# Kernel tuning notes

Hardware: AMD Instinct MI355X
Metric: run time of the kernel (lower is better)

## Reference

```python
import jax, jax.numpy as jnp
import numpy as np

B, S, E, H = 2, 2048, 1024, 16
D = E // H  # d_k = n_wires = 64


def setup_inputs() -> dict:
    key = jax.random.key(0)
    ks = jax.random.split(key, 6)
    x = jax.random.normal(ks[0], (B, S, E), dtype=jnp.float32)
    scale = 0.02
    Wq = jax.random.normal(ks[1], (E, E), dtype=jnp.float32) * scale
    Wk = jax.random.normal(ks[2], (E, E), dtype=jnp.float32) * scale
    Wv = jax.random.normal(ks[3], (E, E), dtype=jnp.float32) * scale
    Wc = jax.random.normal(ks[4], (E, E), dtype=jnp.float32) * scale
    bc = jnp.zeros((E,), dtype=jnp.float32)
    return {"x": x, "Wq": Wq, "Wk": Wk, "Wv": Wv, "Wc": Wc, "bc": bc}


def _split_heads(t):
    # [B,S,E] -> [B,H,S,D]
    return t.reshape(B, S, H, D).transpose(0, 2, 1, 3)


def _quantum(t):
    # RX(theta_i) per wire + CNOT ladder + per-wire PauliZ expectation:
    # <Z_j> = prod_{i<=j} cos(theta_i)  (closed form of the circuit)
    return jnp.cumprod(jnp.cos(t), axis=-1)


def reference(x, Wq, Wk, Wv, Wc, bc):
    q = _quantum(_split_heads(x @ Wq.T))  # [B,H,S,D]
    k = _quantum(_split_heads(x @ Wk.T))
    v = _quantum(_split_heads(x @ Wv.T))
    scores = jnp.einsum('bhsd,bhtd->bhst', q, k) / jnp.sqrt(jnp.float32(D))
    attn = jax.nn.softmax(scores, axis=-1)
    out = jnp.einsum('bhst,bhtd->bhsd', attn, v)  # [B,H,S,D]
    out = out.transpose(0, 2, 1, 3).reshape(B, S, E)
    return out @ Wc.T + bc
```

## Files before the change

kernel.cpp:

```cpp
#include <hip/hip_runtime.h>
#include <hip/hip_bf16.h>

constexpr int Bc = 2, Sc = 2048, Ec = 1024, Hc = 16, Dc = 64;
constexpr int Mrows = Bc * Sc;
constexpr int Kdim  = Ec;

typedef float  floatx4 __attribute__((ext_vector_type(4)));
typedef short  shortx8 __attribute__((ext_vector_type(8)));

__device__ inline unsigned short f2bf(float f) {
    union { __hip_bfloat16 h; unsigned short u; } cv;
    cv.h = __float2bfloat16(f);
    return cv.u;
}

__device__ inline float exp2_fast(float x) {
#if __has_builtin(__builtin_amdgcn_exp2f)
    return __builtin_amdgcn_exp2f(x);
#else
    return __expf(x * 0.69314718056f);
#endif
}

__global__ __launch_bounds__(256) void convert_all_kernel(
    const float* __restrict__ x,  const float* __restrict__ Wq,
    const float* __restrict__ Wk, const float* __restrict__ Wv,
    const float* __restrict__ Wc,
    unsigned short* __restrict__ xb,  unsigned short* __restrict__ Wqb,
    unsigned short* __restrict__ Wkb, unsigned short* __restrict__ Wvb,
    unsigned short* __restrict__ Wcb)
{
    const long t = (long)blockIdx.x * 256 + threadIdx.x;
    const long i = t * 4;
    const float* src; unsigned short* dst; long off;
    if (i < 4194304) { src = x; dst = xb; off = i; }
    else {
        long j = i - 4194304;
        int wsel = (int)(j >> 20);
        off = j & 1048575;
        src = (wsel == 0) ? Wq : (wsel == 1) ? Wk : (wsel == 2) ? Wv : Wc;
        dst = (wsel == 0) ? Wqb : (wsel == 1) ? Wkb : (wsel == 2) ? Wvb : Wcb;
    }
    float4 v = *(const float4*)(src + off);
    unsigned short tmp[4] __attribute__((aligned(8)));
    tmp[0] = f2bf(v.x); tmp[1] = f2bf(v.y); tmp[2] = f2bf(v.z); tmp[3] = f2bf(v.w);
    *(uint2*)(dst + off) = *(uint2*)tmp;
}

__global__ __launch_bounds__(256) void proj_mfma_kernel(
    const unsigned short* __restrict__ Ab,
    const unsigned short* __restrict__ Wqb,
    const unsigned short* __restrict__ Wkb,
    const unsigned short* __restrict__ Wvb,
    unsigned short* __restrict__ oq,
    unsigned short* __restrict__ ok,
    unsigned short* __restrict__ ov)
{
    __shared__ __align__(16) char smem[128 * 72 * 2 * 2];
    unsigned short (*As)[72] = (unsigned short(*)[72])smem;
    unsigned short (*Ws)[72] = (unsigned short(*)[72])(smem + 128 * 72 * 2);
    float (*Cs)[132] = (float(*)[132])smem;
    __shared__ float Sp[64][9];

    const int z = blockIdx.z;
    const unsigned short* Wb = (z == 0) ? Wqb : (z == 1) ? Wkb : Wvb;
    unsigned short* out      = (z == 0) ? oq  : (z == 1) ? ok  : ov;
    const int mode = (z == 2) ? 1 : 0;

    const int tid = threadIdx.x;
    const int w = tid >> 6, l15 = tid & 15, quad = (tid >> 4) & 3;
    const int wq = w >> 1, wn = w & 1;
    const int m0 = blockIdx.x * 128;
    const int n0 = blockIdx.y * 128;
    const int h0 = n0 >> 6;
    const int srow = tid >> 3, schk = tid & 7;

    floatx4 acc[4][4];
    #pragma unroll
    for (int ms = 0; ms < 4; ++ms)
        #pragma unroll
        for (int ns = 0; ns < 4; ++ns)
            #pragma unroll
            for (int e = 0; e < 4; ++e) acc[ms][ns][e] = 0.0f;

    for (int k0 = 0; k0 < Kdim; k0 += 64) {
        #pragma unroll
        for (int it = 0; it < 4; ++it) {
            int row = srow + 32 * it;
            *(shortx8*)&As[row][schk * 8] =
                *(const shortx8*)(Ab + (size_t)(m0 + row) * Kdim + k0 + schk * 8);
            *(shortx8*)&Ws[row][schk * 8] =
                *(const shortx8*)(Wb + (size_t)(n0 + row) * Kdim + k0 + schk * 8);
        }
        __syncthreads();
        #pragma unroll
        for (int ks = 0; ks < 2; ++ks) {
            shortx8 af[4], bf[4];
            #pragma unroll
            for (int ms = 0; ms < 4; ++ms)
                af[ms] = *(shortx8*)&As[64 * wq + 16 * ms + l15][32 * ks + 8 * quad];
            #pragma unroll
            for (int ns = 0; ns < 4; ++ns)
                bf[ns] = *(shortx8*)&Ws[64 * wn + 16 * ns + l15][32 * ks + 8 * quad];
            #pragma unroll
            for (int ms = 0; ms < 4; ++ms)
                #pragma unroll
                for (int ns = 0; ns < 4; ++ns)
                    acc[ms][ns] = __builtin_amdgcn_mfma_f32_16x16x32_bf16(
                        af[ms], bf[ns], acc[ms][ns], 0, 0, 0);
        }
        __syncthreads();
    }

    const int b = m0 >> 11;
    const int sbase = m0 & (Sc - 1);

    for (int pass = 0; pass < 2; ++pass) {
        if (wq == pass) {
            #pragma unroll
            for (int ms = 0; ms < 4; ++ms)
                #pragma unroll
                for (int ns = 0; ns < 4; ++ns)
                    #pragma unroll
                    for (int r = 0; r < 4; ++r)
                        Cs[16 * ms + 4 * quad + r][64 * wn + 16 * ns + l15] =
                            __cosf(acc[ms][ns][r]);
        }
        __syncthreads();
        #pragma unroll
        for (int t = tid; t < 512; t += 256) {
            int row = t >> 3, seg = t & 7;
            float pr = 1.0f;
            #pragma unroll
            for (int c = 0; c < 16; ++c) pr *= Cs[row][seg * 16 + c];
            Sp[row][seg] = pr;
        }
        __syncthreads();
        if (mode == 0) {
            #pragma unroll
            for (int t = tid; t < 512; t += 256) {
                int row = t >> 3, seg = t & 7;
                float p = 1.0f;
                for (int j = (seg & 4); j < seg; ++j) p *= Sp[row][j];
                unsigned short tmp[16] __attribute__((aligned(16)));
                #pragma unroll
                for (int c = 0; c < 16; ++c) { p *= Cs[row][seg * 16 + c]; tmp[c] = f2bf(p); }
                int h = h0 + (seg >> 2);
                int s = sbase + pass * 64 + row;
                size_t base = (((size_t)b * Hc + h) * Sc + s) * Dc + (seg & 3) * 16;
                *(shortx8*)(out + base)     = *(shortx8*)&tmp[0];
                *(shortx8*)(out + base + 8) = *(shortx8*)&tmp[8];
            }
            __syncthreads();
        } else {
            #pragma unroll
            for (int t = tid; t < 512; t += 256) {
                int row = t >> 3, seg = t & 7;
                float p = 1.0f;
                for (int j = (seg & 4); j < seg; ++j) p *= Sp[row][j];
                #pragma unroll
                for (int c = 0; c < 16; ++c) { p *= Cs[row][seg * 16 + c]; Cs[row][seg * 16 + c] = p; }
            }
            __syncthreads();
            #pragma unroll
            for (int t = tid; t < 512; t += 256) {
                int col = t >> 2, chunk = t & 3;
                int h = h0 + (col >> 6), d = col & 63;
                unsigned short tmp[16] __attribute__((aligned(16)));
                #pragma unroll
                for (int j = 0; j < 16; ++j) tmp[j] = f2bf(Cs[chunk * 16 + j][col]);
                size_t base = (((size_t)b * Hc + h) * Dc + d) * Sc
                              + sbase + pass * 64 + chunk * 16;
                *(shortx8*)(out + base)     = *(shortx8*)&tmp[0];
                *(shortx8*)(out + base + 8) = *(shortx8*)&tmp[8];
            }
            __syncthreads();
        }
    }
}

__global__ __launch_bounds__(256) void attn_mfma_kernel(
    const unsigned short* __restrict__ qg,
    const unsigned short* __restrict__ kg,
    const unsigned short* __restrict__ vtg,
    unsigned short* __restrict__ att)
{
    __shared__ __align__(16) unsigned short Ks[64][72];
    __shared__ __align__(16) unsigned short VTs[64][72];
    __shared__ __align__(16) unsigned short Pq[128][72];

    const int tid  = threadIdx.x;
    const int w    = tid >> 6;
    const int l15  = tid & 15;
    const int quad = (tid >> 4) & 3;
    const int qb   = blockIdx.x;
    const int bh   = blockIdx.y;

    const unsigned short* qp = qg  + (size_t)bh * Sc * Dc;
    const unsigned short* kp = kg  + (size_t)bh * Sc * Dc;
    const unsigned short* vp = vtg + (size_t)bh * Dc * Sc;

    int qrow[2];
    shortx8 qf[2][2];
    #pragma unroll
    for (int qs = 0; qs < 2; ++qs) {
        qrow[qs] = qb * 128 + 32 * w + 16 * qs + l15;
        qf[qs][0] = *(const shortx8*)(qp + (size_t)qrow[qs] * Dc + 8 * quad);
        qf[qs][1] = *(const shortx8*)(qp + (size_t)qrow[qs] * Dc + 32 + 8 * quad);
    }

    floatx4 Oacc[2][4];
    #pragma unroll
    for (int qs = 0; qs < 2; ++qs)
        #pragma unroll
        for (int mt = 0; mt < 4; ++mt)
            #pragma unroll
            for (int e = 0; e < 4; ++e) Oacc[qs][mt][e] = 0.0f;
    float lsum[2] = {0.0f, 0.0f};

    const int srow = tid >> 3, schk = tid & 7;
    const float cexp = 0.125f * 1.442695041f;

    for (int kt = 0; kt < Sc / 64; ++kt) {
        #pragma unroll
        for (int it = 0; it < 2; ++it) {
            int row = srow + 32 * it;
            *(shortx8*)&Ks[row][schk * 8] =
                *(const shortx8*)(kp + (size_t)(kt * 64 + row) * Dc + schk * 8);
            *(shortx8*)&VTs[row][schk * 8] =
                *(const shortx8*)(vp + (size_t)row * Sc + kt * 64 + schk * 8);
        }
        __syncthreads();

        shortx8 kf[2][4], vf[2][4];
        #pragma unroll
        for (int ks = 0; ks < 2; ++ks)
            #pragma unroll
            for (int mt = 0; mt < 4; ++mt) {
                kf[ks][mt] = *(shortx8*)&Ks[16 * mt + l15][32 * ks + 8 * quad];
                vf[ks][mt] = *(shortx8*)&VTs[16 * mt + l15][32 * ks + 8 * quad];
            }

        #pragma unroll
        for (int qs = 0; qs < 2; ++qs) {
            floatx4 st[4];
            #pragma unroll
            for (int mt = 0; mt < 4; ++mt)
                #pragma unroll
                for (int e = 0; e < 4; ++e) st[mt][e] = 0.0f;
            #pragma unroll
            for (int ks = 0; ks < 2; ++ks)
                #pragma unroll
                for (int mt = 0; mt < 4; ++mt)
                    st[mt] = __builtin_amdgcn_mfma_f32_16x16x32_bf16(
                        kf[ks][mt], qf[qs][ks], st[mt], 0, 0, 0);

            float rs = 0.0f;
            #pragma unroll
            for (int mt = 0; mt < 4; ++mt) {
                float p0 = exp2_fast(st[mt][0] * cexp);
                float p1 = exp2_fast(st[mt][1] * cexp);
                float p2 = exp2_fast(st[mt][2] * cexp);
                float p3 = exp2_fast(st[mt][3] * cexp);
                rs += (p0 + p1) + (p2 + p3);
                unsigned short tmp[4] __attribute__((aligned(8)));
                tmp[0] = f2bf(p0); tmp[1] = f2bf(p1); tmp[2] = f2bf(p2); tmp[3] = f2bf(p3);
                *(uint2*)&Pq[32 * w + 16 * qs + l15][16 * mt + 4 * quad] = *(uint2*)tmp;
            }
            lsum[qs] += rs;

            #pragma unroll
            for (int ks = 0; ks < 2; ++ks) {
                shortx8 pf = *(shortx8*)&Pq[32 * w + 16 * qs + l15][32 * ks + 8 * quad];
                #pragma unroll
                for (int mt = 0; mt < 4; ++mt)
                    Oacc[qs][mt] = __builtin_amdgcn_mfma_f32_16x16x32_bf16(
                        vf[ks][mt], pf, Oacc[qs][mt], 0, 0, 0);
            }
        }
        __syncthreads();
    }

    const int b = bh >> 4, hh = bh & 15;
    #pragma unroll
    for (int qs = 0; qs < 2; ++qs) {
        float l = lsum[qs];
        l += __shfl_xor(l, 16, 64);
        l += __shfl_xor(l, 32, 64);
        const float inv = 1.0f / l;
        #pragma unroll
        for (int mt = 0; mt < 4; ++mt) {
            unsigned short tmp[4] __attribute__((aligned(8)));
            #pragma unroll
            for (int r = 0; r < 4; ++r) tmp[r] = f2bf(Oacc[qs][mt][r] * inv);
            size_t base = ((size_t)b * Sc + qrow[qs]) * Ec + hh * 64 + 16 * mt + 4 * quad;
            *(uint2*)(att + base) = *(uint2*)tmp;
        }
    }
}

__global__ __launch_bounds__(256) void outproj_mfma_kernel(
    const unsigned short* __restrict__ Ab,
    const unsigned short* __restrict__ Wb,
    const float* __restrict__ bias,
    float* __restrict__ out)
{
    __shared__ __align__(16) unsigned short As[64][72];
    __shared__ __align__(16) unsigned short Ws[128][72];

    const int tid = threadIdx.x;
    const int w = tid >> 6, l15 = tid & 15, quad = (tid >> 4) & 3;
    const int wq = w >> 1, wn = w & 1;
    const int m0 = blockIdx.x * 64;
    const int n0 = blockIdx.y * 128;
    const int srow = tid >> 3, schk = tid & 7;

    floatx4 acc[2][4];
    #pragma unroll
    for (int ms = 0; ms < 2; ++ms)
        #pragma unroll
        for (int ns = 0; ns < 4; ++ns)
            #pragma unroll
            for (int e = 0; e < 4; ++e) acc[ms][ns][e] = 0.0f;

    for (int k0 = 0; k0 < Kdim; k0 += 64) {
        #pragma unroll
        for (int it = 0; it < 2; ++it) {
            int row = srow + 32 * it;
            *(shortx8*)&As[row][schk * 8] =
                *(const shortx8*)(Ab + (size_t)(m0 + row) * Kdim + k0 + schk * 8);
        }
        #pragma unroll
        for (int it = 0; it < 4; ++it) {
            int row = srow + 32 * it;
            *(shortx8*)&Ws[row][schk * 8] =
                *(const shortx8*)(Wb + (size_t)(n0 + row) * Kdim + k0 + schk * 8);
        }
        __syncthreads();
        #pragma unroll
        for (int ks = 0; ks < 2; ++ks) {
            shortx8 af[2], bf[4];
            #pragma unroll
            for (int ms = 0; ms < 2; ++ms)
                af[ms] = *(shortx8*)&As[32 * wq + 16 * ms + l15][32 * ks + 8 * quad];
            #pragma unroll
            for (int ns = 0; ns < 4; ++ns)
                bf[ns] = *(shortx8*)&Ws[64 * wn + 16 * ns + l15][32 * ks + 8 * quad];
            #pragma unroll
            for (int ms = 0; ms < 2; ++ms)
                #pragma unroll
                for (int ns = 0; ns < 4; ++ns)
                    acc[ms][ns] = __builtin_amdgcn_mfma_f32_16x16x32_bf16(
                        af[ms], bf[ns], acc[ms][ns], 0, 0, 0);
        }
        __syncthreads();
    }

    #pragma unroll
    for (int ns = 0; ns < 4; ++ns) {
        const float bv = bias[n0 + 64 * wn + 16 * ns + l15];
        #pragma unroll
        for (int ms = 0; ms < 2; ++ms)
            #pragma unroll
            for (int r = 0; r < 4; ++r) {
                int m = m0 + 32 * wq + 16 * ms + 4 * quad + r;
                out[(size_t)m * Kdim + n0 + 64 * wn + 16 * ns + l15] = acc[ms][ns][r] + bv;
            }
    }
}

extern "C" void kernel_launch(void* const* d_in, const int* in_sizes, int n_in,
                              void* d_out, int out_size, void* d_ws, size_t ws_size,
                              hipStream_t stream) {
    const float* x  = (const float*)d_in[0];
    const float* Wq = (const float*)d_in[1];
    const float* Wk = (const float*)d_in[2];
    const float* Wv = (const float*)d_in[3];
    const float* Wc = (const float*)d_in[4];
    const float* bc = (const float*)d_in[5];
    float* out = (float*)d_out;

    char* p = (char*)d_ws;
    unsigned short* xb   = (unsigned short*)(p);
    unsigned short* Wqb  = (unsigned short*)(p + (8u << 20));
    unsigned short* Wkb  = (unsigned short*)(p + (10u << 20));
    unsigned short* Wvb  = (unsigned short*)(p + (12u << 20));
    unsigned short* Wcb  = (unsigned short*)(p + (14u << 20));
    unsigned short* qb_  = (unsigned short*)(p + (16u << 20));
    unsigned short* kb_  = (unsigned short*)(p + (24u << 20));
    unsigned short* vtb  = (unsigned short*)(p + (32u << 20));
    unsigned short* attb = (unsigned short*)(p + (40u << 20));

    hipLaunchKernelGGL(convert_all_kernel, dim3(8192), dim3(256), 0, stream,
                       x, Wq, Wk, Wv, Wc, xb, Wqb, Wkb, Wvb, Wcb);

    hipLaunchKernelGGL(proj_mfma_kernel, dim3(Mrows / 128, Ec / 128, 3), dim3(256), 0, stream,
                       xb, Wqb, Wkb, Wvb, qb_, kb_, vtb);

    hipLaunchKernelGGL(attn_mfma_kernel, dim3(Sc / 128, Bc * Hc), dim3(256), 0, stream,
                       qb_, kb_, vtb, attb);

    hipLaunchKernelGGL(outproj_mfma_kernel, dim3(Mrows / 64, Ec / 128), dim3(256), 0, stream,
                       attb, Wcb, bc, out);
}
```

Baseline: 228.6 us.

## Use direct global-to-LDS loads with XOR swizzle and split attention over KV halves

The projection, attention and output GEMM kernels now stage tiles with global_load_lds into unpadded LDS tiles, using an XOR-swizzled chunk layout to avoid bank conflicts. This drops the register round-trip and padding. Attention is split into two KV halves per query block, doubling the grid, and each half writes unnormalized partial outputs and row sums. A new combine kernel adds the halves and normalizes them, which costs an extra launch and extra memory traffic. The split relies on the softmax having no running max, and it reuses workspace regions that earlier kernels have finished with.

```diff
diff --git a/kernel.cpp b/kernel.cpp
--- a/kernel.cpp
+++ b/kernel.cpp
@@ -13,13 +13,21 @@
     cv.h = __float2bfloat16(f);
     return cv.u;
 }
-
+__device__ inline float bf2f(unsigned short u) {
+    union { unsigned int i; float f; } c; c.i = ((unsigned int)u) << 16; return c.f;
+}
 __device__ inline float exp2_fast(float x) {
 #if __has_builtin(__builtin_amdgcn_exp2f)
     return __builtin_amdgcn_exp2f(x);
 #else
     return __expf(x * 0.69314718056f);
 #endif
+}
+
+__device__ __forceinline__ void gll16(const void* g, void* lds) {
+    __builtin_amdgcn_global_load_lds(
+        (const __attribute__((address_space(1))) void*)g,
+        (__attribute__((address_space(3))) void*)lds, 16, 0, 0);
 }
 
 __global__ __launch_bounds__(256) void convert_all_kernel(
@@ -56,9 +64,7 @@
     unsigned short* __restrict__ ok,
     unsigned short* __restrict__ ov)
 {
-    __shared__ __align__(16) char smem[128 * 72 * 2 * 2];
-    unsigned short (*As)[72] = (unsigned short(*)[72])smem;
-    unsigned short (*Ws)[72] = (unsigned short(*)[72])(smem + 128 * 72 * 2);
+    __shared__ __align__(16) char smem[33792];
     float (*Cs)[132] = (float(*)[132])smem;
     __shared__ float Sp[64][9];
 
@@ -68,12 +74,13 @@
     const int mode = (z == 2) ? 1 : 0;
 
     const int tid = threadIdx.x;
+    const int lane = tid & 63;
     const int w = tid >> 6, l15 = tid & 15, quad = (tid >> 4) & 3;
     const int wq = w >> 1, wn = w & 1;
     const int m0 = blockIdx.x * 128;
     const int n0 = blockIdx.y * 128;
     const int h0 = n0 >> 6;
-    const int srow = tid >> 3, schk = tid & 7;
+    const int sw = l15 & 7;
 
     floatx4 acc[4][4];
     #pragma unroll
@@ -85,12 +92,14 @@
 
     for (int k0 = 0; k0 < Kdim; k0 += 64) {
         #pragma unroll
-        for (int it = 0; it < 4; ++it) {
-            int row = srow + 32 * it;
-            *(shortx8*)&As[row][schk * 8] =
-                *(const shortx8*)(Ab + (size_t)(m0 + row) * Kdim + k0 + schk * 8);
-            *(shortx8*)&Ws[row][schk * 8] =
-                *(const shortx8*)(Wb + (size_t)(n0 + row) * Kdim + k0 + schk * 8);
+        for (int j = 0; j < 4; ++j) {
+            int idx = j * 64 + lane;
+            int row = 32 * w + (idx >> 3);
+            int cg  = ((idx & 7) ^ (idx >> 3)) & 7;
+            gll16(Ab + (size_t)(m0 + row) * Kdim + k0 + cg * 8,
+                  smem + 4096 * w + 1024 * j);
+            gll16(Wb + (size_t)(n0 + row) * Kdim + k0 + cg * 8,
+                  smem + 16384 + 4096 * w + 1024 * j);
         }
         __syncthreads();
         #pragma unroll
@@ -98,10 +107,12 @@
             shortx8 af[4], bf[4];
             #pragma unroll
             for (int ms = 0; ms < 4; ++ms)
-                af[ms] = *(shortx8*)&As[64 * wq + 16 * ms + l15][32 * ks + 8 * quad];
+                af[ms] = *(shortx8*)(smem + (64 * wq + 16 * ms + l15) * 128
+                                     + (((4 * ks + quad) ^ sw) << 4));
             #pragma unroll
             for (int ns = 0; ns < 4; ++ns)
-                bf[ns] = *(shortx8*)&Ws[64 * wn + 16 * ns + l15][32 * ks + 8 * quad];
+                bf[ns] = *(shortx8*)(smem + 16384 + (64 * wn + 16 * ns + l15) * 128
+                                     + (((4 * ks + quad) ^ sw) << 4));
             #pragma unroll
             for (int ms = 0; ms < 4; ++ms)
                 #pragma unroll
@@ -183,18 +194,22 @@
     const unsigned short* __restrict__ qg,
     const unsigned short* __restrict__ kg,
     const unsigned short* __restrict__ vtg,
-    unsigned short* __restrict__ att)
+    unsigned short* __restrict__ o1,
+    unsigned short* __restrict__ o2,
+    float* __restrict__ lpart)
 {
-    __shared__ __align__(16) unsigned short Ks[64][72];
-    __shared__ __align__(16) unsigned short VTs[64][72];
-    __shared__ __align__(16) unsigned short Pq[128][72];
+    __shared__ __align__(16) char smem[34816];
+    unsigned short (*Pq)[72] = (unsigned short(*)[72])(smem + 16384);
 
     const int tid  = threadIdx.x;
+    const int lane = tid & 63;
     const int w    = tid >> 6;
     const int l15  = tid & 15;
     const int quad = (tid >> 4) & 3;
     const int qb   = blockIdx.x;
-    const int bh   = blockIdx.y;
+    const int half = blockIdx.y;
+    const int bh   = blockIdx.z;
+    const int sw   = l15 & 7;
 
     const unsigned short* qp = qg  + (size_t)bh * Sc * Dc;
     const unsigned short* kp = kg  + (size_t)bh * Sc * Dc;
@@ -218,17 +233,18 @@
             for (int e = 0; e < 4; ++e) Oacc[qs][mt][e] = 0.0f;
     float lsum[2] = {0.0f, 0.0f};
 
-    const int srow = tid >> 3, schk = tid & 7;
     const float cexp = 0.125f * 1.442695041f;
 
-    for (int kt = 0; kt < Sc / 64; ++kt) {
-        #pragma unroll
-        for (int it = 0; it < 2; ++it) {
-            int row = srow + 32 * it;
-            *(shortx8*)&Ks[row][schk * 8] =
-                *(const shortx8*)(kp + (size_t)(kt * 64 + row) * Dc + schk * 8);
-            *(shortx8*)&VTs[row][schk * 8] =
-                *(const shortx8*)(vp + (size_t)row * Sc + kt * 64 + schk * 8);
+    for (int kt = half * 16; kt < half * 16 + 16; ++kt) {
+        #pragma unroll
+        for (int j = 0; j < 2; ++j) {
+            int idx = j * 64 + lane;
+            int row = 16 * w + (idx >> 3);
+            int cg  = ((idx & 7) ^ (idx >> 3)) & 7;
+            gll16(kp + (size_t)(kt * 64 + row) * Dc + cg * 8,
+                  smem + 2048 * w + 1024 * j);
+            gll16(vp + (size_t)row * Sc + kt * 64 + cg * 8,
+                  smem + 8192 + 2048 * w + 1024 * j);
         }
         __syncthreads();
 
@@ -237,8 +253,9 @@
         for (int ks = 0; ks < 2; ++ks)
             #pragma unroll
             for (int mt = 0; mt < 4; ++mt) {
-                kf[ks][mt] = *(shortx8*)&Ks[16 * mt + l15][32 * ks + 8 * quad];
-                vf[ks][mt] = *(shortx8*)&VTs[16 * mt + l15][32 * ks + 8 * quad];
+                int off = (16 * mt + l15) * 128 + (((4 * ks + quad) ^ sw) << 4);
+                kf[ks][mt] = *(shortx8*)(smem + off);
+                vf[ks][mt] = *(shortx8*)(smem + 8192 + off);
             }
 
         #pragma unroll
@@ -282,21 +299,49 @@
     }
 
     const int b = bh >> 4, hh = bh & 15;
+    unsigned short* opart = half ? o2 : o1;
+    float* lp = lpart + ((size_t)half * (Bc * Hc) + bh) * Sc;
     #pragma unroll
     for (int qs = 0; qs < 2; ++qs) {
         float l = lsum[qs];
         l += __shfl_xor(l, 16, 64);
         l += __shfl_xor(l, 32, 64);
-        const float inv = 1.0f / l;
+        if (quad == 0) lp[qrow[qs]] = l;
         #pragma unroll
         for (int mt = 0; mt < 4; ++mt) {
             unsigned short tmp[4] __attribute__((aligned(8)));
             #pragma unroll
-            for (int r = 0; r < 4; ++r) tmp[r] = f2bf(Oacc[qs][mt][r] * inv);
+            for (int r = 0; r < 4; ++r) tmp[r] = f2bf(Oacc[qs][mt][r]);
             size_t base = ((size_t)b * Sc + qrow[qs]) * Ec + hh * 64 + 16 * mt + 4 * quad;
-            *(uint2*)(att + base) = *(uint2*)tmp;
-        }
-    }
+            *(uint2*)(opart + base) = *(uint2*)tmp;
+        }
+    }
+}
+
+__global__ __launch_bounds__(256) void combine_kernel(
+    unsigned short* __restrict__ o1,
+    const unsigned short* __restrict__ o2,
+    const float* __restrict__ lpart)
+{
+    const size_t t = (size_t)blockIdx.x * 256 + threadIdx.x;
+    const size_t base = t * 8;
+    const int e = (int)(base & (Ec - 1));
+    const int h = e >> 6;
+    const size_t bs = base >> 10;
+    const int b = (int)(bs >> 11), s = (int)(bs & (Sc - 1));
+    const int bh = b * Hc + h;
+    const float l = lpart[(size_t)bh * Sc + s]
+                  + lpart[(size_t)(Bc * Hc + bh) * Sc + s];
+    const float inv = 1.0f / l;
+    uint4 a = *(const uint4*)(o1 + base);
+    uint4 c = *(const uint4*)(o2 + base);
+    const unsigned short* ua = (const unsigned short*)&a;
+    const unsigned short* uc = (const unsigned short*)&c;
+    unsigned short r[8] __attribute__((aligned(16)));
+    #pragma unroll
+    for (int i = 0; i < 8; ++i)
+        r[i] = f2bf((bf2f(ua[i]) + bf2f(uc[i])) * inv);
+    *(uint4*)(o1 + base) = *(uint4*)r;
 }
 
 __global__ __launch_bounds__(256) void outproj_mfma_kernel(
@@ -305,15 +350,15 @@
     const float* __restrict__ bias,
     float* __restrict__ out)
 {
-    __shared__ __align__(16) unsigned short As[64][72];
-    __shared__ __align__(16) unsigned short Ws[128][72];
+    __shared__ __align__(16) char smem[24576];
 
     const int tid = threadIdx.x;
+    const int lane = tid & 63;
     const int w = tid >> 6, l15 = tid & 15, quad = (tid >> 4) & 3;
     const int wq = w >> 1, wn = w & 1;
     const int m0 = blockIdx.x * 64;
     const int n0 = blockIdx.y * 128;
-    const int srow = tid >> 3, schk = tid & 7;
+    const int sw = l15 & 7;
 
     floatx4 acc[2][4];
     #pragma unroll
@@ -325,16 +370,20 @@
 
     for (int k0 = 0; k0 < Kdim; k0 += 64) {
         #pragma unroll
-        for (int it = 0; it < 2; ++it) {
-            int row = srow + 32 * it;
-            *(shortx8*)&As[row][schk * 8] =
-                *(const shortx8*)(Ab + (size_t)(m0 + row) * Kdim + k0 + schk * 8);
-        }
-        #pragma unroll
-        for (int it = 0; it < 4; ++it) {
-            int row = srow + 32 * it;
-            *(shortx8*)&Ws[row][schk * 8] =
-                *(const shortx8*)(Wb + (size_t)(n0 + row) * Kdim + k0 + schk * 8);
+        for (int j = 0; j < 2; ++j) {
+            int idx = j * 64 + lane;
+            int row = 16 * w + (idx >> 3);
+            int cg  = ((idx & 7) ^ (idx >> 3)) & 7;
+            gll16(Ab + (size_t)(m0 + row) * Kdim + k0 + cg * 8,
+                  smem + 2048 * w + 1024 * j);
+        }
+        #pragma unroll
+        for (int j = 0; j < 4; ++j) {
+            int idx = j * 64 + lane;
+            int row = 32 * w + (idx >> 3);
+            int cg  = ((idx & 7) ^ (idx >> 3)) & 7;
+            gll16(Wb + (size_t)(n0 + row) * Kdim + k0 + cg * 8,
+                  smem + 8192 + 4096 * w + 1024 * j);
         }
         __syncthreads();
         #pragma unroll
@@ -342,10 +391,12 @@
             shortx8 af[2], bf[4];
             #pragma unroll
             for (int ms = 0; ms < 2; ++ms)
-                af[ms] = *(shortx8*)&As[32 * wq + 16 * ms + l15][32 * ks + 8 * quad];
+                af[ms] = *(shortx8*)(smem + (32 * wq + 16 * ms + l15) * 128
+                                     + (((4 * ks + quad) ^ sw) << 4));
             #pragma unroll
             for (int ns = 0; ns < 4; ++ns)
-                bf[ns] = *(shortx8*)&Ws[64 * wn + 16 * ns + l15][32 * ks + 8 * quad];
+                bf[ns] = *(shortx8*)(smem + 8192 + (64 * wn + 16 * ns + l15) * 128
+                                     + (((4 * ks + quad) ^ sw) << 4));
             #pragma unroll
             for (int ms = 0; ms < 2; ++ms)
                 #pragma unroll
@@ -390,6 +441,8 @@
     unsigned short* kb_  = (unsigned short*)(p + (24u << 20));
     unsigned short* vtb  = (unsigned short*)(p + (32u << 20));
     unsigned short* attb = (unsigned short*)(p + (40u << 20));
+    unsigned short* o2b  = xb;
+    float*          lpart = (float*)(p + (8u << 20));
 
     hipLaunchKernelGGL(convert_all_kernel, dim3(8192), dim3(256), 0, stream,
                        x, Wq, Wk, Wv, Wc, xb, Wqb, Wkb, Wvb, Wcb);
@@ -397,8 +450,11 @@
     hipLaunchKernelGGL(proj_mfma_kernel, dim3(Mrows / 128, Ec / 128, 3), dim3(256), 0, stream,
                        xb, Wqb, Wkb, Wvb, qb_, kb_, vtb);
 
-    hipLaunchKernelGGL(attn_mfma_kernel, dim3(Sc / 128, Bc * Hc), dim3(256), 0, stream,
-                       qb_, kb_, vtb, attb);
+    hipLaunchKernelGGL(attn_mfma_kernel, dim3(Sc / 128, 2, Bc * Hc), dim3(256), 0, stream,
+                       qb_, kb_, vtb, attb, o2b, lpart);
+
+    hipLaunchKernelGGL(combine_kernel, dim3(Mrows * Ec / (256 * 8)), dim3(256), 0, stream,
+                       attb, o2b, lpart);
 
     hipLaunchKernelGGL(outproj_mfma_kernel, dim3(Mrows / 64, Ec / 128), dim3(256), 0, stream,
                        attb, Wcb, bc, out);
```

New measurement: 212.8 us. 6.9% less time.
